# Performance work log

Hardware: AMD Instinct MI355X
Metric: run time of the kernel (lower is better)

The kernel has to match this reference:

```python
import jax, jax.numpy as jnp
import numpy as np

B, C, W = 16, 256, 64


def qlinear(x, Wm, b):
    # x: (b, Cin, 4); Wm: (4, Cout, Cin); b: (4, Cout)
    # Separate linear per quaternion component, then Hamilton-like combine.
    comps = jnp.einsum('bic,coi->boc', x, Wm) + b.T[None]  # (b, Cout, 4)
    r, xc, yc, zc = comps[..., 0], comps[..., 1], comps[..., 2], comps[..., 3]
    return jnp.stack([
        r + xc + yc + zc,
        xc - r - zc + yc,
        yc + zc - r - xc,
        zc - yc + xc - r,
    ], axis=-1)  # (b, Cout, 4)


def setup_inputs() -> dict:
    key = jax.random.key(0)
    k0, k1, k2, k3, k4 = jax.random.split(key, 5)
    return {
        'x': jax.random.normal(k0, (B, C, W, W, 4), dtype=jnp.float32),
        'comp_w': jax.random.normal(k1, (4, 1, C), dtype=jnp.float32) * (1.0 / np.sqrt(C)),
        'comp_b': jax.random.normal(k2, (4, 1), dtype=jnp.float32) * 0.01,
        'exc_w': jax.random.normal(k3, (4, C, 1), dtype=jnp.float32),
        'exc_b': jax.random.normal(k4, (4, C), dtype=jnp.float32) * 0.01,
    }


def reference(x, comp_w, comp_b, exc_w, exc_b):
    # Global max pool over spatial dims, per quaternion component: (b, C, 4)
    pooled = jnp.max(x, axis=(2, 3))
    u = qlinear(pooled, comp_w, comp_b)          # (b, 1, 4)
    u = qlinear(u, exc_w, exc_b)                 # (b, C, 4)
    # Broadcast per-channel, per-component scale over spatial dims
    return x * u[:, :, None, None, :]
```

## Files before the change

### kernel.cpp

```cpp
#include <hip/hip_runtime.h>

#define B 16
#define C 256
#define SPATIAL 4096

__global__ __launch_bounds__(256) void pool_kernel(const float4* __restrict__ x4,
                                                   float4* __restrict__ pooled4) {
    const int bc = blockIdx.x;
    const float4* p = x4 + (size_t)bc * SPATIAL;
    const int tid = threadIdx.x;

    float4 m = p[tid];
    #pragma unroll
    for (int s = tid + 256; s < SPATIAL; s += 256) {
        float4 v = p[s];
        m.x = fmaxf(m.x, v.x);
        m.y = fmaxf(m.y, v.y);
        m.z = fmaxf(m.z, v.z);
        m.w = fmaxf(m.w, v.w);
    }

    #pragma unroll
    for (int off = 32; off > 0; off >>= 1) {
        m.x = fmaxf(m.x, __shfl_down(m.x, off));
        m.y = fmaxf(m.y, __shfl_down(m.y, off));
        m.z = fmaxf(m.z, __shfl_down(m.z, off));
        m.w = fmaxf(m.w, __shfl_down(m.w, off));
    }

    __shared__ float4 lm[4];
    const int lane = tid & 63, wid = tid >> 6;
    if (lane == 0) lm[wid] = m;
    __syncthreads();
    if (tid == 0) {
        float4 r = lm[0];
        #pragma unroll
        for (int w = 1; w < 4; ++w) {
            r.x = fmaxf(r.x, lm[w].x);
            r.y = fmaxf(r.y, lm[w].y);
            r.z = fmaxf(r.z, lm[w].z);
            r.w = fmaxf(r.w, lm[w].w);
        }
        pooled4[bc] = r;
    }
}

__global__ __launch_bounds__(256) void scale_kernel(const float4* __restrict__ pooled4,
                                                    const float* __restrict__ comp_w,
                                                    const float* __restrict__ comp_b,
                                                    const float* __restrict__ exc_w,
                                                    const float* __restrict__ exc_b,
                                                    float4* __restrict__ scale4) {
    const int b = blockIdx.x;
    const int o = threadIdx.x;

    float4 p = pooled4[b * C + o];
    float4 prod;
    prod.x = p.x * comp_w[0 * C + o];
    prod.y = p.y * comp_w[1 * C + o];
    prod.z = p.z * comp_w[2 * C + o];
    prod.w = p.w * comp_w[3 * C + o];

    #pragma unroll
    for (int off = 32; off > 0; off >>= 1) {
        prod.x += __shfl_down(prod.x, off);
        prod.y += __shfl_down(prod.y, off);
        prod.z += __shfl_down(prod.z, off);
        prod.w += __shfl_down(prod.w, off);
    }

    __shared__ float4 lsum[4];
    const int lane = o & 63, wid = o >> 6;
    if (lane == 0) lsum[wid] = prod;
    __syncthreads();

    float r  = lsum[0].x + lsum[1].x + lsum[2].x + lsum[3].x + comp_b[0];
    float xc = lsum[0].y + lsum[1].y + lsum[2].y + lsum[3].y + comp_b[1];
    float yc = lsum[0].z + lsum[1].z + lsum[2].z + lsum[3].z + comp_b[2];
    float zc = lsum[0].w + lsum[1].w + lsum[2].w + lsum[3].w + comp_b[3];

    const float u0 = r + xc + yc + zc;
    const float u1 = xc - r - zc + yc;
    const float u2 = yc + zc - r - xc;
    const float u3 = zc - yc + xc - r;

    const float c0 = u0 * exc_w[0 * C + o] + exc_b[0 * C + o];
    const float c1 = u1 * exc_w[1 * C + o] + exc_b[1 * C + o];
    const float c2 = u2 * exc_w[2 * C + o] + exc_b[2 * C + o];
    const float c3 = u3 * exc_w[3 * C + o] + exc_b[3 * C + o];

    float4 s;
    s.x = c0 + c1 + c2 + c3;
    s.y = c1 - c0 - c3 + c2;
    s.z = c2 + c3 - c0 - c1;
    s.w = c3 - c2 + c1 - c0;
    scale4[b * C + o] = s;
}

__global__ __launch_bounds__(256) void mul_kernel(const float4* __restrict__ x4,
                                                  const float4* __restrict__ scale4,
                                                  float4* __restrict__ out4) {
    const int bc = blockIdx.x;
    const float4 s = scale4[bc];
    const float4* xp = x4 + (size_t)bc * SPATIAL;
    float4* op = out4 + (size_t)bc * SPATIAL;
    #pragma unroll 4
    for (int i = threadIdx.x; i < SPATIAL; i += 256) {
        float4 v = xp[i];
        v.x *= s.x;
        v.y *= s.y;
        v.z *= s.z;
        v.w *= s.w;
        op[i] = v;
    }
}

extern "C" void kernel_launch(void* const* d_in, const int* in_sizes, int n_in,
                              void* d_out, int out_size, void* d_ws, size_t ws_size,
                              hipStream_t stream) {
    const float4* x4     = (const float4*)d_in[0];
    const float*  comp_w = (const float*)d_in[1];
    const float*  comp_b = (const float*)d_in[2];
    const float*  exc_w  = (const float*)d_in[3];
    const float*  exc_b  = (const float*)d_in[4];
    float4* out4 = (float4*)d_out;

    float4* pooled4 = (float4*)d_ws;
    float4* scale4  = pooled4 + B * C;

    pool_kernel<<<B * C, 256, 0, stream>>>(x4, pooled4);
    scale_kernel<<<B, 256, 0, stream>>>(pooled4, comp_w, comp_b, exc_w, exc_b, scale4);
    mul_kernel<<<B * C, 256, 0, stream>>>(x4, scale4, out4);
}
```

Baseline: 495.9 us.

## Fuse scale computation into multiply kernel with reversed block order and nontemporal stores

Removes the separate tiny scale kernel by having every multiply block recompute its batch's squeeze-excite scale from the pooled values. Blocks are processed in reverse order, so the most recently pooled (likely cache-resident) slices of x are read first. Output is written with nontemporal stores to avoid polluting cache. In exchange, the small reduction is redundantly repeated 256 times per batch, and one launch plus a dependency gap is saved.

Result: faster. 482.2 us (-2.8%).

```diff
diff --git a/kernel.cpp b/kernel.cpp
--- a/kernel.cpp
+++ b/kernel.cpp
@@ -3,6 +3,8 @@
 #define B 16
 #define C 256
 #define SPATIAL 4096
+
+typedef float vf4 __attribute__((ext_vector_type(4)));
 
 __global__ __launch_bounds__(256) void pool_kernel(const float4* __restrict__ x4,
                                                    float4* __restrict__ pooled4) {
@@ -45,21 +47,24 @@
     }
 }
 
-__global__ __launch_bounds__(256) void scale_kernel(const float4* __restrict__ pooled4,
-                                                    const float* __restrict__ comp_w,
-                                                    const float* __restrict__ comp_b,
-                                                    const float* __restrict__ exc_w,
-                                                    const float* __restrict__ exc_b,
-                                                    float4* __restrict__ scale4) {
-    const int b = blockIdx.x;
-    const int o = threadIdx.x;
+__global__ __launch_bounds__(256) void scale_mul_kernel(const float4* __restrict__ x4,
+                                                        const float4* __restrict__ pooled4,
+                                                        const float* __restrict__ comp_w,
+                                                        const float* __restrict__ comp_b,
+                                                        const float* __restrict__ exc_w,
+                                                        const float* __restrict__ exc_b,
+                                                        float4* __restrict__ out4) {
+    const int bc  = (B * C - 1) - blockIdx.x;
+    const int b   = bc >> 8;
+    const int c   = bc & (C - 1);
+    const int tid = threadIdx.x;
 
-    float4 p = pooled4[b * C + o];
+    float4 p = pooled4[b * C + tid];
     float4 prod;
-    prod.x = p.x * comp_w[0 * C + o];
-    prod.y = p.y * comp_w[1 * C + o];
-    prod.z = p.z * comp_w[2 * C + o];
-    prod.w = p.w * comp_w[3 * C + o];
+    prod.x = p.x * comp_w[0 * C + tid];
+    prod.y = p.y * comp_w[1 * C + tid];
+    prod.z = p.z * comp_w[2 * C + tid];
+    prod.w = p.w * comp_w[3 * C + tid];
 
     #pragma unroll
     for (int off = 32; off > 0; off >>= 1) {
@@ -70,48 +75,38 @@
     }
 
     __shared__ float4 lsum[4];
-    const int lane = o & 63, wid = o >> 6;
+    const int lane = tid & 63, wid = tid >> 6;
     if (lane == 0) lsum[wid] = prod;
     __syncthreads();
 
-    float r  = lsum[0].x + lsum[1].x + lsum[2].x + lsum[3].x + comp_b[0];
-    float xc = lsum[0].y + lsum[1].y + lsum[2].y + lsum[3].y + comp_b[1];
-    float yc = lsum[0].z + lsum[1].z + lsum[2].z + lsum[3].z + comp_b[2];
-    float zc = lsum[0].w + lsum[1].w + lsum[2].w + lsum[3].w + comp_b[3];
+    const float r  = lsum[0].x + lsum[1].x + lsum[2].x + lsum[3].x + comp_b[0];
+    const float xc = lsum[0].y + lsum[1].y + lsum[2].y + lsum[3].y + comp_b[1];
+    const float yc = lsum[0].z + lsum[1].z + lsum[2].z + lsum[3].z + comp_b[2];
+    const float zc = lsum[0].w + lsum[1].w + lsum[2].w + lsum[3].w + comp_b[3];
 
     const float u0 = r + xc + yc + zc;
     const float u1 = xc - r - zc + yc;
     const float u2 = yc + zc - r - xc;
     const float u3 = zc - yc + xc - r;
 
-    const float c0 = u0 * exc_w[0 * C + o] + exc_b[0 * C + o];
-    const float c1 = u1 * exc_w[1 * C + o] + exc_b[1 * C + o];
-    const float c2 = u2 * exc_w[2 * C + o] + exc_b[2 * C + o];
-    const float c3 = u3 * exc_w[3 * C + o] + exc_b[3 * C + o];
+    const float c0 = u0 * exc_w[0 * C + c] + exc_b[0 * C + c];
+    const float c1 = u1 * exc_w[1 * C + c] + exc_b[1 * C + c];
+    const float c2 = u2 * exc_w[2 * C + c] + exc_b[2 * C + c];
+    const float c3 = u3 * exc_w[3 * C + c] + exc_b[3 * C + c];
 
-    float4 s;
+    vf4 s;
     s.x = c0 + c1 + c2 + c3;
     s.y = c1 - c0 - c3 + c2;
     s.z = c2 + c3 - c0 - c1;
     s.w = c3 - c2 + c1 - c0;
-    scale4[b * C + o] = s;
-}
 
-__global__ __launch_bounds__(256) void mul_kernel(const float4* __restrict__ x4,
-                                                  const float4* __restrict__ scale4,
-                                                  float4* __restrict__ out4) {
-    const int bc = blockIdx.x;
-    const float4 s = scale4[bc];
-    const float4* xp = x4 + (size_t)bc * SPATIAL;
-    float4* op = out4 + (size_t)bc * SPATIAL;
+    const vf4* xp = (const vf4*)(x4 + (size_t)bc * SPATIAL);
+    vf4*       op = (vf4*)(out4 + (size_t)bc * SPATIAL);
     #pragma unroll 4
-    for (int i = threadIdx.x; i < SPATIAL; i += 256) {
-        float4 v = xp[i];
-        v.x *= s.x;
-        v.y *= s.y;
-        v.z *= s.z;
-        v.w *= s.w;
-        op[i] = v;
+    for (int i = tid; i < SPATIAL; i += 256) {
+        vf4 v = xp[i];
+        v *= s;
+        __builtin_nontemporal_store(v, op + i);
     }
 }
 
@@ -126,9 +121,8 @@
     float4* out4 = (float4*)d_out;
 
     float4* pooled4 = (float4*)d_ws;
-    float4* scale4  = pooled4 + B * C;
 
     pool_kernel<<<B * C, 256, 0, stream>>>(x4, pooled4);
-    scale_kernel<<<B, 256, 0, stream>>>(pooled4, comp_w, comp_b, exc_w, exc_b, scale4);
-    mul_kernel<<<B * C, 256, 0, stream>>>(x4, scale4, out4);
+    scale_mul_kernel<<<B * C, 256, 0, stream>>>(x4, pooled4, comp_w, comp_b,
+                                                exc_w, exc_b, out4);
 }
```
